# Performance work log

Hardware: AMD Instinct MI355X
Metric: run time of the kernel (lower is better)

Reference implementation:

```python
import jax, jax.numpy as jnp
import numpy as np

B, P, C, H, W = 256, 512, 512, 7, 8
T = H * W  # 56
EPS = 1e-8


def setup_inputs() -> dict:
    key = jax.random.key(0)
    k1, k2, k3 = jax.random.split(key, 3)
    inp = jax.random.normal(k1, (B, C, H, W), dtype=jnp.float32)
    # xavier-uniform-like init for prototype (fan over last two dims as torch does)
    bound_p = float(np.sqrt(6.0 / (P + C * T)))
    prototype = jax.random.uniform(k2, (P, C, T), dtype=jnp.float32, minval=-bound_p, maxval=bound_p)
    bound_w = float(np.sqrt(6.0 / (C + 1)))
    fc_w = jax.random.uniform(k3, (1, C), dtype=jnp.float32, minval=-bound_w, maxval=bound_w)
    fc_b = jnp.zeros((1,), dtype=jnp.float32)
    return {"input": inp, "prototype": prototype, "fc_w": fc_w, "fc_b": fc_b}


def reference(input, prototype, fc_w, fc_b):
    # flatten spatial dims: (B, C, T)
    x = input.reshape(input.shape[0], input.shape[1], -1)
    # per-position cosine similarity over channel dim
    dots = jnp.einsum('bct,pct->bpt', x, prototype)          # (B, P, T)
    xn = jnp.linalg.norm(x, axis=1)                           # (B, T)
    pn = jnp.linalg.norm(prototype, axis=1)                   # (P, T)
    sim = dots / jnp.maximum(xn[:, None, :] * pn[None, :, :], EPS)
    att = jax.nn.softmax(sim, axis=-1)                        # (B, P, T)
    # attention-pooled elementwise product: (B, P, C)
    feat = jnp.einsum('bpt,bct,pct->bpc', att, x, prototype)
    # fc: Linear(C, 1) then relu, view to (B, P)
    out = jax.nn.relu(jnp.einsum('bpc,oc->bpo', feat, fc_w) + fc_b)
    return out.reshape(out.shape[0], out.shape[1])
```

## Files before the change

kernel.cpp:

```cpp
#include <hip/hip_runtime.h>
#include <hip/hip_bf16.h>
#include <math.h>

constexpr int kB = 256, kC = 512, kT = 56, kP = 512;
constexpr int kCT = kC * kT;

typedef short v4s __attribute__((ext_vector_type(4)));
typedef short v8s __attribute__((ext_vector_type(8)));
typedef float v4f __attribute__((ext_vector_type(4)));
typedef float v16f __attribute__((ext_vector_type(16)));

__device__ __forceinline__ unsigned pack_bf16(float a, float b) {
  __hip_bfloat16 ha = __float2bfloat16(a);
  __hip_bfloat16 hb = __float2bfloat16(b);
  unsigned short ua, ub;
  __builtin_memcpy(&ua, &ha, 2);
  __builtin_memcpy(&ub, &hb, 2);
  return (unsigned)ua | ((unsigned)ub << 16);
}

__device__ __forceinline__ v4s frag2(unsigned w0, unsigned w1) {
  unsigned u[2] = {w0, w1};
  v4s s;
  __builtin_memcpy(&s, u, 8);
  return s;
}

__device__ __forceinline__ v8s frag8(uint4 u) {
  v8s s;
  __builtin_memcpy(&s, &u, 16);
  return s;
}

__device__ __forceinline__ float bfl(unsigned u) {
  unsigned v = u << 16;
  float f;
  __builtin_memcpy(&f, &v, 4);
  return f;
}
__device__ __forceinline__ float bfh(unsigned u) {
  unsigned v = u & 0xffff0000u;
  float f;
  __builtin_memcpy(&f, &v, 4);
  return f;
}
__device__ __forceinline__ unsigned cvtpk(float lo, float hi) {
  unsigned r;
  asm("v_cvt_pk_bf16_f32 %0, %1, %2" : "=v"(r) : "v"(lo), "v"(hi));
  return r;
}

__global__ __launch_bounds__(512) void prep_kernel(
    const float* __restrict__ x, const float* __restrict__ proto,
    unsigned* __restrict__ xt, unsigned* __restrict__ pt,
    float* __restrict__ xn, float* __restrict__ pn) {
  __shared__ float tile[128 * 57];
  __shared__ float part[8][64];

  const int tid = threadIdx.x;
  const int n = blockIdx.x;
  const bool isx = (n < kB);
  const int row = isx ? n : (n - kB);
  const float* src = (isx ? x : proto) + (size_t)row * kCT;

  const int g = tid >> 6, tt = tid & 63;
  float nacc = 0.f;

#pragma unroll 1
  for (int ch = 0; ch < 4; ++ch) {
    const float* csrc = src + ch * (128 * 56);
#pragma unroll
    for (int it = 0; it < 4; ++it) {
      const int idx = it * 512 + tid;
      if (idx < 1792) {
        const int f0 = idx * 4;
        float4 v = *(const float4*)(csrc + f0);
        int c = (int)(((unsigned)f0 * 74899u) >> 22);
        int t = f0 - c * 56;
        tile[c * 57 + t] = v.x;
        tile[c * 57 + t + 1] = v.y;
        tile[c * 57 + t + 2] = v.z;
        tile[c * 57 + t + 3] = v.w;
      }
    }
    __syncthreads();
    if (tt < 56) {
#pragma unroll
      for (int cc2 = 0; cc2 < 16; ++cc2) {
        float u = tile[(g * 16 + cc2) * 57 + tt];
        nacc = fmaf(u, u, nacc);
      }
    }
#pragma unroll
    for (int it = 0; it < 7; ++it) {
      const int id = it * 512 + tid;
      const int t = id >> 6;
      const int cw = id & 63;
      float g0 = tile[(2 * cw) * 57 + t];
      float g1 = tile[(2 * cw + 1) * 57 + t];
      unsigned wd = pack_bf16(g0, g1);
      if (isx)
        xt[((size_t)(t * kB + row)) * 256 + ch * 64 + cw] = wd;
      else
        pt[((size_t)(t * kP + row)) * 256 + ch * 64 + cw] = wd;
    }
    __syncthreads();
  }

  part[g][tt] = nacc;
  __syncthreads();
  if (tid < 56) {
    float s = 0.f;
#pragma unroll
    for (int gg = 0; gg < 8; ++gg) s += part[gg][tid];
    float r = sqrtf(s);
    if (isx) xn[row * 56 + tid] = r; else pn[row * 56 + tid] = r;
  }
}

constexpr int CW = 32;
constexpr int TILE = 64 * CW;
constexpr int BUFW = 3 * TILE;

__global__ __launch_bounds__(256, 3) void proto_gemm_kernel(
    const unsigned* __restrict__ xt, const unsigned* __restrict__ pt,
    const float* __restrict__ fcw,
    const float* __restrict__ xn, const float* __restrict__ pn,
    float* __restrict__ part) {
  __shared__ __align__(16) unsigned lds[2 * BUFW];

  const int tid = threadIdx.x;
  const int l = tid & 63;
  const int w = tid >> 6;
  const int wm = w >> 1;
  const int wn = w & 1;
  const int b0 = blockIdx.x * 64;
  const int p0 = blockIdx.y * 64;
  const int tg = blockIdx.z;

  const int srow = tid >> 3;
  const int scolw = (tid & 7) * 4;
  const int ssw = (srow & 7) * 4;
  const int lwA = srow * CW + (scolw ^ ssw);
  const int lwB = (srow + 32) * CW + (scolw ^ ssw);

  const int fr = l & 31;
  const int hi = l >> 5;
  const int sw4 = (l & 7) * 4;
  const int axb = (wm * 32 + fr) * CW;
  const int pxb = (wn * 32 + fr) * CW;

  v16f aD, aW, sac, nac;
#pragma unroll
  for (int i = 0; i < 16; ++i) { aD[i] = 0.f; aW[i] = 0.f; sac[i] = 0.f; nac[i] = 0.f; }

  uint4 Ax0, Ax1, Ap0, Ap1;
  float4 Af0, Af1;
  uint4 Bx0, Bx1, Bp0, Bp1;
  float4 Bf0, Bf1;

#define LOAD_REGS(S, CC) do { \
    const int t_ = tg * 4 + ((CC) >> 3); \
    const int ch_ = (CC) & 7; \
    const unsigned* gx_ = xt + ((size_t)(t_ * kB + b0 + srow)) * 256 + ch_ * CW + scolw; \
    const unsigned* gp_ = pt + ((size_t)(t_ * kP + p0 + srow)) * 256 + ch_ * CW + scolw; \
    S##x0 = *(const uint4*)(gx_); \
    S##x1 = *(const uint4*)(gx_ + 32 * 256); \
    S##p0 = *(const uint4*)(gp_); \
    S##p1 = *(const uint4*)(gp_ + 32 * 256); \
    const float* gf_ = fcw + ch_ * 64 + (tid & 7) * 8; \
    S##f0 = *(const float4*)(gf_); \
    S##f1 = *(const float4*)(gf_ + 4); \
  } while (0)

#define WMUL(xv, fa, fb, out) do { \
    out.x = cvtpk(bfl(xv.x) * fa.x, bfh(xv.x) * fa.y); \
    out.y = cvtpk(bfl(xv.y) * fa.z, bfh(xv.y) * fa.w); \
    out.z = cvtpk(bfl(xv.z) * fb.x, bfh(xv.z) * fb.y); \
    out.w = cvtpk(bfl(xv.w) * fb.z, bfh(xv.w) * fb.w); \
  } while (0)

#define STORE_LDS(S, CC) do { \
    unsigned* b_ = lds + ((CC) & 1) * BUFW; \
    *(uint4*)(b_ + lwA) = S##x0; \
    *(uint4*)(b_ + lwB) = S##x1; \
    uint4 w0_, w1_; \
    WMUL(S##x0, S##f0, S##f1, w0_); \
    WMUL(S##x1, S##f0, S##f1, w1_); \
    *(uint4*)(b_ + TILE + lwA) = w0_; \
    *(uint4*)(b_ + TILE + lwB) = w1_; \
    *(uint4*)(b_ + 2 * TILE + lwA) = S##p0; \
    *(uint4*)(b_ + 2 * TILE + lwB) = S##p1; \
  } while (0)

  auto compute = [&](int cc) {
    const unsigned* bx = lds + (cc & 1) * BUFW;
#pragma unroll
    for (int ks = 0; ks < 4; ++ks) {
      const int col = (ks * 8 + hi * 4) ^ sw4;
      uint4 xr = *(const uint4*)(bx + axb + col);
      uint4 wr = *(const uint4*)(bx + TILE + axb + col);
      uint4 pr = *(const uint4*)(bx + 2 * TILE + pxb + col);
      v8s xf = frag8(xr), wf = frag8(wr), pf = frag8(pr);
      aD = __builtin_amdgcn_mfma_f32_32x32x16_bf16(xf, pf, aD, 0, 0, 0);
      aW = __builtin_amdgcn_mfma_f32_32x32x16_bf16(wf, pf, aW, 0, 0, 0);
    }
    if ((cc & 7) == 7) {
      const int t = tg * 4 + (cc >> 3);
      const float pnv = pn[(p0 + wn * 32 + fr) * 56 + t];
#pragma unroll
      for (int i = 0; i < 16; ++i) {
        const int drow = (i & 3) + 8 * (i >> 2) + 4 * hi;
        float xnv = xn[(b0 + wm * 32 + drow) * 56 + t];
        float den = fmaxf(xnv * pnv, 1e-8f);
        float sim = aD[i] * __builtin_amdgcn_rcpf(den);
        float e = __expf(sim);
        sac[i] += e;
        nac[i] = fmaf(e, aW[i], nac[i]);
        aD[i] = 0.f;
        aW[i] = 0.f;
      }
    }
  };

  LOAD_REGS(A, 0);
  STORE_LDS(A, 0);
  LOAD_REGS(B, 1);
  __syncthreads();

#pragma unroll 1
  for (int cc = 0; cc < 32; cc += 2) {
    if (cc + 1 < 32) STORE_LDS(B, cc + 1);
    if (cc + 2 < 32) LOAD_REGS(A, cc + 2);
    compute(cc);
    __syncthreads();
    if (cc + 2 < 32) STORE_LDS(A, cc + 2);
    if (cc + 3 < 32) LOAD_REGS(B, cc + 3);
    compute(cc + 1);
    __syncthreads();
  }

#undef LOAD_REGS
#undef WMUL
#undef STORE_LDS

  float* psb = part + ((size_t)tg * 2 + 0) * 131072;
  float* pnb = part + ((size_t)tg * 2 + 1) * 131072;
#pragma unroll
  for (int i = 0; i < 16; ++i) {
    const int drow = (i & 3) + 8 * (i >> 2) + 4 * hi;
    const size_t o = (size_t)(b0 + wm * 32 + drow) * 512 + p0 + wn * 32 + fr;
    psb[o] = sac[i];
    pnb[o] = nac[i];
  }
}

__global__ __launch_bounds__(256) void merge_kernel(
    const float* __restrict__ part, const float* __restrict__ fcb,
    float* __restrict__ out) {
  const int pair = blockIdx.x * 256 + threadIdx.x;
  float S = 0.f, N = 0.f;
#pragma unroll
  for (int k = 0; k < 14; ++k) {
    S += part[((size_t)k * 2 + 0) * 131072 + pair];
    N += part[((size_t)k * 2 + 1) * 131072 + pair];
  }
  float o = N * __builtin_amdgcn_rcpf(S) + fcb[0];
  out[pair] = fmaxf(o, 0.f);
}

__global__ __launch_bounds__(1024) void proto_mfma_kernel(
    const float* __restrict__ x, const float* __restrict__ proto,
    const float* __restrict__ fcw, const float* __restrict__ fcb,
    float* __restrict__ out) {
  __shared__ unsigned xs[56 * 289];
  __shared__ unsigned ps[56 * 145];
  __shared__ unsigned pws[56 * 145];

  const int tid = threadIdx.x;
  const int l = tid & 63;
  const int w = tid >> 6;
  const int bq = w & 1;
  const int tq = w >> 1;
  const int t0 = tq * 7;

  const int n = blockIdx.y * 32 + blockIdx.x;
  const int p0 = (n >> 3) * 16;
  const int b0 = (n & 7) * 32;

  const bool act = (l < 56);
  const int lt = l;

  const int xbase0 = ((b0 + 2 * w + 0) * kC) * kT + lt;
  const int xbase1 = ((b0 + 2 * w + 1) * kC) * kT + lt;
  const int pbase = ((p0 + w) * kC) * kT + lt;

  const int arow = l & 15;
  const int q2 = (l >> 4) << 1;
  const int xoff = (bq * 16 + arow) * 9 + q2;
  const int poff = arow * 9 + q2;

  v4f acc[7][2];
#pragma unroll
  for (int ti = 0; ti < 7; ++ti) {
    acc[ti][0] = v4f{0.f, 0.f, 0.f, 0.f};
    acc[ti][1] = v4f{0.f, 0.f, 0.f, 0.f};
  }
  float xn2a = 0.f, xn2b = 0.f, pn2 = 0.f;

#pragma unroll 1
  for (int st = 0; st < 32; ++st) {
    const int k0 = st * 16;
    if (act) {
#pragma unroll
      for (int r = 0; r < 16; ++r) {
        const int cw = r & 7;
        const int c = k0 + 2 * cw;
        const int ga = ((r >> 3) ? xbase1 : xbase0) + c * kT;
        float g0 = x[ga], g1 = x[ga + kT];
        if (r >> 3) xn2b = fmaf(g0, g0, fmaf(g1, g1, xn2b));
        else xn2a = fmaf(g0, g0, fmaf(g1, g1, xn2a));
        xs[lt * 289 + (2 * w + (r >> 3)) * 9 + cw] = pack_bf16(g0, g1);
      }
#pragma unroll
      for (int cw = 0; cw < 8; ++cw) {
        const int c = k0 + 2 * cw;
        const int ga = pbase + c * kT;
        float g0 = proto[ga], g1 = proto[ga + kT];
        pn2 = fmaf(g0, g0, fmaf(g1, g1, pn2));
        ps[lt * 145 + w * 9 + cw] = pack_bf16(g0, g1);
        float f0 = fcw[c], f1 = fcw[c + 1];
        pws[lt * 145 + w * 9 + cw] = pack_bf16(g0 * f0, g1 * f1);
      }
    }
    __syncthreads();
#pragma unroll
    for (int ti = 0; ti < 7; ++ti) {
      const int t = t0 + ti;
      unsigned xw0 = xs[t * 289 + xoff];
      unsigned xw1 = xs[t * 289 + xoff + 1];
      unsigned pw0 = ps[t * 145 + poff];
      unsigned pw1 = ps[t * 145 + poff + 1];
      unsigned ww0 = pws[t * 145 + poff];
      unsigned ww1 = pws[t * 145 + poff + 1];
      v4s af = frag2(xw0, xw1);
      v4s bf = frag2(pw0, pw1);
      v4s wf = frag2(ww0, ww1);
      acc[ti][0] = __builtin_amdgcn_mfma_f32_16x16x16bf16_1k(af, bf, acc[ti][0], 0, 0, 0);
      acc[ti][1] = __builtin_amdgcn_mfma_f32_16x16x16bf16_1k(af, wf, acc[ti][1], 0, 0, 0);
    }
    __syncthreads();
  }

  float* xnorm = (float*)ps;
  float* pnorm = xnorm + 32 * 56;
  if (act) {
    xnorm[(2 * w + 0) * 56 + lt] = xn2a;
    xnorm[(2 * w + 1) * 56 + lt] = xn2b;
    pnorm[w * 56 + lt] = pn2;
  }
  __syncthreads();

  float* fm = (float*)xs;
  float* fsum = fm + 4096;
  float* fnum = fsum + 4096;
  const int pc = arow;
  const int qq = l >> 4;
#pragma unroll
  for (int i = 0; i < 4; ++i) {
    const int bl = bq * 16 + 4 * qq + i;
    float m = -3.0e38f;
    float sims[7];
#pragma unroll
    for (int ti = 0; ti < 7; ++ti) {
      const int t = t0 + ti;
      float den = fmaxf(sqrtf(xnorm[bl * 56 + t]) * sqrtf(pnorm[pc * 56 + t]), 1e-8f);
      float s = acc[ti][0][i] / den;
      sims[ti] = s;
      m = fmaxf(m, s);
    }
    float se = 0.f, nu = 0.f;
#pragma unroll
    for (int ti = 0; ti < 7; ++ti) {
      float e = __expf(sims[ti] - m);
      se += e;
      nu = fmaf(e, acc[ti][1][i], nu);
    }
    const int pair = bl * 16 + pc;
    fm[tq * 512 + pair] = m;
    fsum[tq * 512 + pair] = se;
    fnum[tq * 512 + pair] = nu;
  }
  __syncthreads();

  if (tid < 512) {
    float M = -3.0e38f;
#pragma unroll
    for (int k = 0; k < 8; ++k) M = fmaxf(M, fm[k * 512 + tid]);
    float S = 0.f, N = 0.f;
#pragma unroll
    for (int k = 0; k < 8; ++k) {
      float sc = __expf(fm[k * 512 + tid] - M);
      S = fmaf(fsum[k * 512 + tid], sc, S);
      N = fmaf(fnum[k * 512 + tid], sc, N);
    }
    float o = N / S + fcb[0];
    out[(b0 + (tid >> 4)) * kP + p0 + (tid & 15)] = fmaxf(o, 0.f);
  }
}

extern "C" void kernel_launch(void* const* d_in, const int* in_sizes, int n_in,
                              void* d_out, int out_size, void* d_ws, size_t ws_size,
                              hipStream_t stream) {
  const float* x = (const float*)d_in[0];
  const float* proto = (const float*)d_in[1];
  const float* fcw = (const float*)d_in[2];
  const float* fcb = (const float*)d_in[3];
  float* out = (float*)d_out;

  const size_t need = 58892288;
  if (ws_size >= need) {
    unsigned* xt = (unsigned*)d_ws;
    unsigned* ptb = xt + 3670016;
    float* partb = (float*)(xt + 11010048);
    float* xnb = (float*)(xt + 14680064);
    float* pnb = (float*)(xt + 14694400);

    hipLaunchKernelGGL(prep_kernel, dim3(kB + kP), dim3(512), 0, stream,
                       x, proto, xt, ptb, xnb, pnb);
    hipLaunchKernelGGL(proto_gemm_kernel, dim3(4, 8, 14), dim3(256), 0, stream,
                       xt, ptb, fcw, xnb, pnb, partb);
    hipLaunchKernelGGL(merge_kernel, dim3(512), dim3(256), 0, stream,
                       partb, fcb, out);
  } else {
    hipLaunchKernelGGL(proto_mfma_kernel, dim3(32, 8), dim3(1024), 0, stream,
                       x, proto, fcw, fcb, out);
  }
}
```

Measured before the change: 62.38 us.

## Split T into more groups, swizzle block order, stage norms in LDS

The GEMM kernel is templated on time-steps per block, and when the workspace is large enough it launches 28 T-groups of 2 steps instead of 14 groups of 4. That doubles the grid (896 blocks) for better CU occupancy, and the merge kernel reads twice as many partial sums in exchange. Block IDs are remapped so neighbouring blocks land on different XCDs or share operands. The xn/pn norm values are preloaded into LDS instead of being read from global memory inside the softmax epilogue.

```diff
diff --git a/kernel.cpp b/kernel.cpp
--- a/kernel.cpp
+++ b/kernel.cpp
@@ -122,21 +122,33 @@
 constexpr int TILE = 64 * CW;
 constexpr int BUFW = 3 * TILE;
 
+template <int TPB>
 __global__ __launch_bounds__(256, 3) void proto_gemm_kernel(
     const unsigned* __restrict__ xt, const unsigned* __restrict__ pt,
     const float* __restrict__ fcw,
     const float* __restrict__ xn, const float* __restrict__ pn,
     float* __restrict__ part) {
   __shared__ __align__(16) unsigned lds[2 * BUFW];
+  __shared__ float xnL[TPB * 64], pnL[TPB * 64];
 
   const int tid = threadIdx.x;
   const int l = tid & 63;
   const int w = tid >> 6;
   const int wm = w >> 1;
   const int wn = w & 1;
-  const int b0 = blockIdx.x * 64;
-  const int p0 = blockIdx.y * 64;
-  const int tg = blockIdx.z;
+
+  const int nwg = 32 * (56 / TPB);
+  int bid = (int)blockIdx.x + 4 * ((int)blockIdx.y + 8 * (int)blockIdx.z);
+  bid = (bid & 7) * (nwg >> 3) + (bid >> 3);
+  const int b0 = (bid & 3) * 64;
+  const int p0 = ((bid >> 2) & 7) * 64;
+  const int tg = bid >> 5;
+
+  if (tid < TPB * 64) {
+    const int tl = tid >> 6, r = tid & 63;
+    xnL[tl * 64 + r] = xn[(b0 + r) * 56 + tg * TPB + tl];
+    pnL[tl * 64 + r] = pn[(p0 + r) * 56 + tg * TPB + tl];
+  }
 
   const int srow = tid >> 3;
   const int scolw = (tid & 7) * 4;
@@ -160,7 +172,7 @@
   float4 Bf0, Bf1;
 
 #define LOAD_REGS(S, CC) do { \
-    const int t_ = tg * 4 + ((CC) >> 3); \
+    const int t_ = tg * TPB + ((CC) >> 3); \
     const int ch_ = (CC) & 7; \
     const unsigned* gx_ = xt + ((size_t)(t_ * kB + b0 + srow)) * 256 + ch_ * CW + scolw; \
     const unsigned* gp_ = pt + ((size_t)(t_ * kP + p0 + srow)) * 256 + ch_ * CW + scolw; \
@@ -206,12 +218,12 @@
       aW = __builtin_amdgcn_mfma_f32_32x32x16_bf16(wf, pf, aW, 0, 0, 0);
     }
     if ((cc & 7) == 7) {
-      const int t = tg * 4 + (cc >> 3);
-      const float pnv = pn[(p0 + wn * 32 + fr) * 56 + t];
+      const int tl = cc >> 3;
+      const float pnv = pnL[tl * 64 + wn * 32 + fr];
 #pragma unroll
       for (int i = 0; i < 16; ++i) {
         const int drow = (i & 3) + 8 * (i >> 2) + 4 * hi;
-        float xnv = xn[(b0 + wm * 32 + drow) * 56 + t];
+        float xnv = xnL[tl * 64 + wm * 32 + drow];
         float den = fmaxf(xnv * pnv, 1e-8f);
         float sim = aD[i] * __builtin_amdgcn_rcpf(den);
         float e = __expf(sim);
@@ -228,14 +240,15 @@
   LOAD_REGS(B, 1);
   __syncthreads();
 
+  constexpr int NCC = TPB * 8;
 #pragma unroll 1
-  for (int cc = 0; cc < 32; cc += 2) {
-    if (cc + 1 < 32) STORE_LDS(B, cc + 1);
-    if (cc + 2 < 32) LOAD_REGS(A, cc + 2);
+  for (int cc = 0; cc < NCC; cc += 2) {
+    if (cc + 1 < NCC) STORE_LDS(B, cc + 1);
+    if (cc + 2 < NCC) LOAD_REGS(A, cc + 2);
     compute(cc);
     __syncthreads();
-    if (cc + 2 < 32) STORE_LDS(A, cc + 2);
-    if (cc + 3 < 32) LOAD_REGS(B, cc + 3);
+    if (cc + 2 < NCC) STORE_LDS(A, cc + 2);
+    if (cc + 3 < NCC) LOAD_REGS(B, cc + 3);
     compute(cc + 1);
     __syncthreads();
   }
@@ -255,13 +268,14 @@
   }
 }
 
+template <int NG>
 __global__ __launch_bounds__(256) void merge_kernel(
     const float* __restrict__ part, const float* __restrict__ fcb,
     float* __restrict__ out) {
   const int pair = blockIdx.x * 256 + threadIdx.x;
   float S = 0.f, N = 0.f;
 #pragma unroll
-  for (int k = 0; k < 14; ++k) {
+  for (int k = 0; k < NG; ++k) {
     S += part[((size_t)k * 2 + 0) * 131072 + pair];
     N += part[((size_t)k * 2 + 1) * 131072 + pair];
   }
@@ -418,20 +432,30 @@
   const float* fcb = (const float*)d_in[3];
   float* out = (float*)d_out;
 
-  const size_t need = 58892288;
-  if (ws_size >= need) {
+  const size_t need2 = 73572352;
+  const size_t need4 = 58892288;
+  if (ws_size >= need4) {
+    const bool big = (ws_size >= need2);
     unsigned* xt = (unsigned*)d_ws;
     unsigned* ptb = xt + 3670016;
     float* partb = (float*)(xt + 11010048);
-    float* xnb = (float*)(xt + 14680064);
-    float* pnb = (float*)(xt + 14694400);
+    const size_t partw = big ? (size_t)28 * 2 * 131072 : (size_t)14 * 2 * 131072;
+    float* xnb = (float*)(xt + 11010048) + partw;
+    float* pnb = xnb + 14336;
 
     hipLaunchKernelGGL(prep_kernel, dim3(kB + kP), dim3(512), 0, stream,
                        x, proto, xt, ptb, xnb, pnb);
-    hipLaunchKernelGGL(proto_gemm_kernel, dim3(4, 8, 14), dim3(256), 0, stream,
-                       xt, ptb, fcw, xnb, pnb, partb);
-    hipLaunchKernelGGL(merge_kernel, dim3(512), dim3(256), 0, stream,
-                       partb, fcb, out);
+    if (big) {
+      hipLaunchKernelGGL(proto_gemm_kernel<2>, dim3(4, 8, 28), dim3(256), 0, stream,
+                         xt, ptb, fcw, xnb, pnb, partb);
+      hipLaunchKernelGGL(merge_kernel<28>, dim3(512), dim3(256), 0, stream,
+                         partb, fcb, out);
+    } else {
+      hipLaunchKernelGGL(proto_gemm_kernel<4>, dim3(4, 8, 14), dim3(256), 0, stream,
+                         xt, ptb, fcw, xnb, pnb, partb);
+      hipLaunchKernelGGL(merge_kernel<14>, dim3(512), dim3(256), 0, stream,
+                         partb, fcb, out);
+    }
   } else {
     hipLaunchKernelGGL(proto_mfma_kernel, dim3(32, 8), dim3(1024), 0, stream,
                        x, proto, fcw, fcb, out);
```

New measurement: 72.39 us. 16.0% more time.

## Precompute fc-weighted x in prep and stream tiles via global_load_lds

Applied to the files above, without the earlier changes.

The prep kernel now also writes a bf16 copy of x pre-multiplied by the fc weights, so the GEMM kernel no longer unpacks, multiplies and repacks in registers. The GEMM stages tiles straight from global memory into LDS with global_load_lds, using a wider 64-word K tile and a swizzled layout. The grid becomes 256 blocks over 8 time groups of 7, with a remapped block index. Norms are cached in LDS, and the merge kernel reduces 8 partials instead of 14. In exchange, prep writes an extra x-sized buffer, the workspace grows, and fewer, longer-running blocks lower occupancy.

```diff
diff --git a/kernel.cpp b/kernel.cpp
--- a/kernel.cpp
+++ b/kernel.cpp
@@ -32,29 +32,19 @@
   return s;
 }
 
-__device__ __forceinline__ float bfl(unsigned u) {
-  unsigned v = u << 16;
-  float f;
-  __builtin_memcpy(&f, &v, 4);
-  return f;
-}
-__device__ __forceinline__ float bfh(unsigned u) {
-  unsigned v = u & 0xffff0000u;
-  float f;
-  __builtin_memcpy(&f, &v, 4);
-  return f;
-}
-__device__ __forceinline__ unsigned cvtpk(float lo, float hi) {
-  unsigned r;
-  asm("v_cvt_pk_bf16_f32 %0, %1, %2" : "=v"(r) : "v"(lo), "v"(hi));
-  return r;
-}
+#define GLOAD(gp, lp)                                                        \
+  __builtin_amdgcn_global_load_lds(                                          \
+      (const __attribute__((address_space(1))) unsigned*)(const unsigned*)(gp), \
+      (__attribute__((address_space(3))) unsigned*)(unsigned*)(lp), 16, 0, 0)
 
 __global__ __launch_bounds__(512) void prep_kernel(
     const float* __restrict__ x, const float* __restrict__ proto,
-    unsigned* __restrict__ xt, unsigned* __restrict__ pt,
+    const float* __restrict__ fcw,
+    unsigned* __restrict__ xt, unsigned* __restrict__ xwt,
+    unsigned* __restrict__ pt,
     float* __restrict__ xn, float* __restrict__ pn) {
   __shared__ float tile[128 * 57];
+  __shared__ float fws[512];
   __shared__ float part[8][64];
 
   const int tid = threadIdx.x;
@@ -62,6 +52,8 @@
   const bool isx = (n < kB);
   const int row = isx ? n : (n - kB);
   const float* src = (isx ? x : proto) + (size_t)row * kCT;
+
+  fws[tid] = fcw[tid & 511];
 
   const int g = tid >> 6, tt = tid & 63;
   float nacc = 0.f;
@@ -99,10 +91,14 @@
       float g0 = tile[(2 * cw) * 57 + t];
       float g1 = tile[(2 * cw + 1) * 57 + t];
       unsigned wd = pack_bf16(g0, g1);
-      if (isx)
-        xt[((size_t)(t * kB + row)) * 256 + ch * 64 + cw] = wd;
-      else
+      if (isx) {
+        const size_t o = ((size_t)(t * kB + row)) * 256 + ch * 64 + cw;
+        const int c = ch * 128 + 2 * cw;
+        xt[o] = wd;
+        xwt[o] = pack_bf16(g0 * fws[c], g1 * fws[c + 1]);
+      } else {
         pt[((size_t)(t * kP + row)) * 256 + ch * 64 + cw] = wd;
+      }
     }
     __syncthreads();
   }
@@ -118,100 +114,88 @@
   }
 }
 
-constexpr int CW = 32;
-constexpr int TILE = 64 * CW;
+constexpr int TILE = 64 * 64;
 constexpr int BUFW = 3 * TILE;
 
-__global__ __launch_bounds__(256, 3) void proto_gemm_kernel(
-    const unsigned* __restrict__ xt, const unsigned* __restrict__ pt,
-    const float* __restrict__ fcw,
+__global__ __launch_bounds__(256) void proto_gemm_kernel(
+    const unsigned* __restrict__ xt, const unsigned* __restrict__ xwt,
+    const unsigned* __restrict__ pt,
     const float* __restrict__ xn, const float* __restrict__ pn,
     float* __restrict__ part) {
   __shared__ __align__(16) unsigned lds[2 * BUFW];
+  __shared__ float xnL[7 * 64], pnL[7 * 64];
 
   const int tid = threadIdx.x;
   const int l = tid & 63;
-  const int w = tid >> 6;
-  const int wm = w >> 1;
-  const int wn = w & 1;
-  const int b0 = blockIdx.x * 64;
-  const int p0 = blockIdx.y * 64;
-  const int tg = blockIdx.z;
-
-  const int srow = tid >> 3;
-  const int scolw = (tid & 7) * 4;
-  const int ssw = (srow & 7) * 4;
-  const int lwA = srow * CW + (scolw ^ ssw);
-  const int lwB = (srow + 32) * CW + (scolw ^ ssw);
+  const int w4 = tid >> 6;
+  const int wm = w4 >> 1;
+  const int wn = w4 & 1;
+
+  int bid = (int)blockIdx.x;
+  bid = (bid & 7) * 32 + (bid >> 3);
+  const int b0 = (bid & 3) * 64;
+  const int p0 = ((bid >> 2) & 7) * 64;
+  const int tg = bid >> 5;
+
+  for (int i = tid; i < 7 * 64; i += 256) {
+    const int tl = i >> 6, r = i & 63;
+    xnL[i] = xn[(b0 + r) * 56 + tg * 7 + tl];
+    pnL[i] = pn[(p0 + r) * 56 + tg * 7 + tl];
+  }
+
+  const int l16 = l >> 4, s16 = l & 15;
+  size_t xro[4], pro[4];
+  int lo[4];
+#pragma unroll
+  for (int jj = 0; jj < 4; ++jj) {
+    const int row = w4 * 16 + jj * 4 + l16;
+    const int ch4 = (s16 ^ (row & 7)) * 4;
+    xro[jj] = (size_t)(b0 + row) * 256 + ch4;
+    pro[jj] = (size_t)(p0 + row) * 256 + ch4;
+    lo[jj] = (w4 * 16 + jj * 4) * 64;
+  }
 
   const int fr = l & 31;
   const int hi = l >> 5;
   const int sw4 = (l & 7) * 4;
-  const int axb = (wm * 32 + fr) * CW;
-  const int pxb = (wn * 32 + fr) * CW;
+  const int axb = (wm * 32 + fr) * 64;
+  const int pxb = (wn * 32 + fr) * 64;
 
   v16f aD, aW, sac, nac;
 #pragma unroll
   for (int i = 0; i < 16; ++i) { aD[i] = 0.f; aW[i] = 0.f; sac[i] = 0.f; nac[i] = 0.f; }
 
-  uint4 Ax0, Ax1, Ap0, Ap1;
-  float4 Af0, Af1;
-  uint4 Bx0, Bx1, Bp0, Bp1;
-  float4 Bf0, Bf1;
-
-#define LOAD_REGS(S, CC) do { \
-    const int t_ = tg * 4 + ((CC) >> 3); \
-    const int ch_ = (CC) & 7; \
-    const unsigned* gx_ = xt + ((size_t)(t_ * kB + b0 + srow)) * 256 + ch_ * CW + scolw; \
-    const unsigned* gp_ = pt + ((size_t)(t_ * kP + p0 + srow)) * 256 + ch_ * CW + scolw; \
-    S##x0 = *(const uint4*)(gx_); \
-    S##x1 = *(const uint4*)(gx_ + 32 * 256); \
-    S##p0 = *(const uint4*)(gp_); \
-    S##p1 = *(const uint4*)(gp_ + 32 * 256); \
-    const float* gf_ = fcw + ch_ * 64 + (tid & 7) * 8; \
-    S##f0 = *(const float4*)(gf_); \
-    S##f1 = *(const float4*)(gf_ + 4); \
-  } while (0)
-
-#define WMUL(xv, fa, fb, out) do { \
-    out.x = cvtpk(bfl(xv.x) * fa.x, bfh(xv.x) * fa.y); \
-    out.y = cvtpk(bfl(xv.y) * fa.z, bfh(xv.y) * fa.w); \
-    out.z = cvtpk(bfl(xv.z) * fb.x, bfh(xv.z) * fb.y); \
-    out.w = cvtpk(bfl(xv.w) * fb.z, bfh(xv.w) * fb.w); \
-  } while (0)
-
-#define STORE_LDS(S, CC) do { \
-    unsigned* b_ = lds + ((CC) & 1) * BUFW; \
-    *(uint4*)(b_ + lwA) = S##x0; \
-    *(uint4*)(b_ + lwB) = S##x1; \
-    uint4 w0_, w1_; \
-    WMUL(S##x0, S##f0, S##f1, w0_); \
-    WMUL(S##x1, S##f0, S##f1, w1_); \
-    *(uint4*)(b_ + TILE + lwA) = w0_; \
-    *(uint4*)(b_ + TILE + lwB) = w1_; \
-    *(uint4*)(b_ + 2 * TILE + lwA) = S##p0; \
-    *(uint4*)(b_ + 2 * TILE + lwB) = S##p1; \
-  } while (0)
-
-  auto compute = [&](int cc) {
-    const unsigned* bx = lds + (cc & 1) * BUFW;
-#pragma unroll
-    for (int ks = 0; ks < 4; ++ks) {
+  auto STAGE = [&](int s, int buf) {
+    const int t = tg * 7 + (s >> 2);
+    const size_t xoff = (size_t)t * (kB * 256) + (size_t)((s & 3) * 64);
+    const size_t poff = (size_t)t * (kP * 256) + (size_t)((s & 3) * 64);
+    unsigned* lb = lds + buf * BUFW;
+#pragma unroll
+    for (int jj = 0; jj < 4; ++jj) {
+      GLOAD(xt + xro[jj] + xoff, lb + lo[jj]);
+      GLOAD(xwt + xro[jj] + xoff, lb + TILE + lo[jj]);
+      GLOAD(pt + pro[jj] + poff, lb + 2 * TILE + lo[jj]);
+    }
+  };
+
+  auto COMPUTE = [&](int s) {
+    const unsigned* bx = lds + (s & 1) * BUFW;
+#pragma unroll
+    for (int ks = 0; ks < 8; ++ks) {
       const int col = (ks * 8 + hi * 4) ^ sw4;
-      uint4 xr = *(const uint4*)(bx + axb + col);
-      uint4 wr = *(const uint4*)(bx + TILE + axb + col);
-      uint4 pr = *(const uint4*)(bx + 2 * TILE + pxb + col);
-      v8s xf = frag8(xr), wf = frag8(wr), pf = frag8(pr);
+      v8s xf = frag8(*(const uint4*)(bx + axb + col));
+      v8s wf = frag8(*(const uint4*)(bx + TILE + axb + col));
+      v8s pf = frag8(*(const uint4*)(bx + 2 * TILE + pxb + col));
       aD = __builtin_amdgcn_mfma_f32_32x32x16_bf16(xf, pf, aD, 0, 0, 0);
       aW = __builtin_amdgcn_mfma_f32_32x32x16_bf16(wf, pf, aW, 0, 0, 0);
     }
-    if ((cc & 7) == 7) {
-      const int t = tg * 4 + (cc >> 3);
-      const float pnv = pn[(p0 + wn * 32 + fr) * 56 + t];
+    if ((s & 3) == 3) {
+      const int tl = s >> 2;
+      const float pnv = pnL[tl * 64 + wn * 32 + fr];
 #pragma unroll
       for (int i = 0; i < 16; ++i) {
         const int drow = (i & 3) + 8 * (i >> 2) + 4 * hi;
-        float xnv = xn[(b0 + wm * 32 + drow) * 56 + t];
+        float xnv = xnL[tl * 64 + wm * 32 + drow];
         float den = fmaxf(xnv * pnv, 1e-8f);
         float sim = aD[i] * __builtin_amdgcn_rcpf(den);
         float e = __expf(sim);
@@ -223,26 +207,15 @@
     }
   };
 
-  LOAD_REGS(A, 0);
-  STORE_LDS(A, 0);
-  LOAD_REGS(B, 1);
+  STAGE(0, 0);
   __syncthreads();
 
 #pragma unroll 1
-  for (int cc = 0; cc < 32; cc += 2) {
-    if (cc + 1 < 32) STORE_LDS(B, cc + 1);
-    if (cc + 2 < 32) LOAD_REGS(A, cc + 2);
-    compute(cc);
+  for (int s = 0; s < 28; ++s) {
+    if (s < 27) STAGE(s + 1, (s + 1) & 1);
+    COMPUTE(s);
     __syncthreads();
-    if (cc + 2 < 32) STORE_LDS(A, cc + 2);
-    if (cc + 3 < 32) LOAD_REGS(B, cc + 3);
-    compute(cc + 1);
-    __syncthreads();
-  }
-
-#undef LOAD_REGS
-#undef WMUL
-#undef STORE_LDS
+  }
 
   float* psb = part + ((size_t)tg * 2 + 0) * 131072;
   float* pnb = part + ((size_t)tg * 2 + 1) * 131072;
@@ -261,7 +234,7 @@
   const int pair = blockIdx.x * 256 + threadIdx.x;
   float S = 0.f, N = 0.f;
 #pragma unroll
-  for (int k = 0; k < 14; ++k) {
+  for (int k = 0; k < 8; ++k) {
     S += part[((size_t)k * 2 + 0) * 131072 + pair];
     N += part[((size_t)k * 2 + 1) * 131072 + pair];
   }
@@ -418,18 +391,19 @@
   const float* fcb = (const float*)d_in[3];
   float* out = (float*)d_out;
 
-  const size_t need = 58892288;
+  const size_t need = 67280896;
   if (ws_size >= need) {
     unsigned* xt = (unsigned*)d_ws;
-    unsigned* ptb = xt + 3670016;
-    float* partb = (float*)(xt + 11010048);
-    float* xnb = (float*)(xt + 14680064);
-    float* pnb = (float*)(xt + 14694400);
+    unsigned* xwt = xt + 3670016;
+    unsigned* ptb = xt + 7340032;
+    float* partb = (float*)(xt + 14680064);
+    float* xnb = (float*)(xt + 16777216);
+    float* pnb = xnb + 14336;
 
     hipLaunchKernelGGL(prep_kernel, dim3(kB + kP), dim3(512), 0, stream,
-                       x, proto, xt, ptb, xnb, pnb);
-    hipLaunchKernelGGL(proto_gemm_kernel, dim3(4, 8, 14), dim3(256), 0, stream,
-                       xt, ptb, fcw, xnb, pnb, partb);
+                       x, proto, fcw, xt, xwt, ptb, xnb, pnb);
+    hipLaunchKernelGGL(proto_gemm_kernel, dim3(256), dim3(256), 0, stream,
+                       xt, xwt, ptb, xnb, pnb, partb);
     hipLaunchKernelGGL(merge_kernel, dim3(512), dim3(256), 0, stream,
                        partb, fcb, out);
   } else {
```

New measurement: 76.03 us. 21.9% more time.
